# Kernel tuning notes

Hardware: AMD Instinct MI355X
Metric: run time of the kernel (lower is better)

The kernel has to match this reference:

```python
import jax, jax.numpy as jnp
import numpy as np

N = 100000
E = 640000
IN, HID, OUT = 128, 256, 128


def _glorot(key, shape):
    fan_in, fan_out = shape[0], shape[1]
    lim = (6.0 / (fan_in + fan_out)) ** 0.5
    return jax.random.uniform(key, shape, jnp.float32, -lim, lim)


def setup_inputs() -> dict:
    key = jax.random.key(0)
    ks = jax.random.split(key, 8)
    x = jax.random.normal(ks[0], (N, IN), jnp.float32)
    edge_index = jax.random.randint(ks[1], (2, E), 0, N, jnp.int64)
    # conv0 MLP: in->hid->hid
    w0a = _glorot(ks[2], (IN, HID)); b0a = jnp.zeros((HID,), jnp.float32)
    w0b = _glorot(ks[3], (HID, HID)); b0b = jnp.zeros((HID,), jnp.float32)
    # conv1 MLP: hid->hid->hid
    w1a = _glorot(ks[4], (HID, HID)); b1a = jnp.zeros((HID,), jnp.float32)
    w1b = _glorot(ks[5], (HID, HID)); b1b = jnp.zeros((HID,), jnp.float32)
    # conv2 MLP: hid->out->out
    w2a = _glorot(ks[6], (HID, OUT)); b2a = jnp.zeros((OUT,), jnp.float32)
    w2b = _glorot(ks[7], (OUT, OUT)); b2b = jnp.zeros((OUT,), jnp.float32)
    return dict(x=x, edge_index=edge_index,
                w0a=w0a, b0a=b0a, w0b=w0b, b0b=b0b,
                w1a=w1a, b1a=b1a, w1b=w1b, b1b=b1b,
                w2a=w2a, b2a=b2a, w2b=w2b, b2b=b2b)


def reference(x, edge_index, w0a, b0a, w0b, b0b, w1a, b1a, w1b, b1b, w2a, b2a, w2b, b2b):
    src, dst = edge_index[0], edge_index[1]
    n = x.shape[0]
    layers = [(w0a, b0a, w0b, b0b), (w1a, b1a, w1b, b1b), (w2a, b2a, w2b, b2b)]
    for wa, ba, wb, bb in layers:
        # GINConv (eps=0): aggregate neighbor messages x[src] into dst, add self
        agg = jax.ops.segment_sum(x[src], dst, num_segments=n)  # [N, d]
        h = x + agg
        h = jnp.maximum(h @ wa + ba, 0.0) @ wb + bb  # MLP: Linear-ReLU-Linear
        x = jnp.maximum(h, 0.0)  # outer F.relu
    return x
```

## Files before the change

kernel.cpp:

```cpp
#include <hip/hip_runtime.h>
#include <hip/hip_bf16.h>

typedef __attribute__((ext_vector_type(4))) float f32x4;
typedef __attribute__((ext_vector_type(8))) short short8;
typedef unsigned short u16;

__device__ inline float bf2f(u16 u) {
    unsigned int x = ((unsigned int)u) << 16;
    return __builtin_bit_cast(float, x);
}
__device__ inline u16 f2bf(float f) {
    unsigned int x = __builtin_bit_cast(unsigned int, f);
    unsigned int r = (x + 0x7FFFu + ((x >> 16) & 1u)) >> 16;
    return (u16)r;
}

__device__ inline int edge_at(const void* edges, int flag64, long long idx) {
    if (flag64) return (int)((const long long*)edges)[idx];
    return ((const int*)edges)[idx];
}

__global__ void probe_kernel(const void* edges, int n, int* flag) {
    if (threadIdx.x == 0 && blockIdx.x == 0) {
        const long long* p = (const long long*)edges;
        int ok = 1;
        for (int i = 0; i < 64; ++i) {
            long long v = p[i];
            if (v < 0 || v >= n) { ok = 0; break; }
        }
        *flag = ok;
    }
}

__global__ void hist_kernel(const void* edges, const int* flag, int E, int* deg) {
    int f = *flag;
    for (long long i = blockIdx.x * blockDim.x + threadIdx.x; i < E;
         i += (long long)gridDim.x * blockDim.x) {
        int dst = edge_at(edges, f, (long long)E + i);
        atomicAdd(&deg[dst], 1);
    }
}

__global__ void scan1_kernel(const int* deg, int* incl, int* bsum, int n) {
    __shared__ int s[256];
    int i = blockIdx.x * 256 + threadIdx.x;
    int v = (i < n) ? deg[i] : 0;
    s[threadIdx.x] = v;
    __syncthreads();
    for (int d = 1; d < 256; d <<= 1) {
        int t = (threadIdx.x >= d) ? s[threadIdx.x - d] : 0;
        __syncthreads();
        s[threadIdx.x] += t;
        __syncthreads();
    }
    if (i < n) incl[i] = s[threadIdx.x];
    if (threadIdx.x == 255) bsum[blockIdx.x] = s[255];
}

__global__ void scan2_kernel(const int* bsum, int* boff, int nb) {
    __shared__ int s[512];
    int t = threadIdx.x;
    int v = (t < nb) ? bsum[t] : 0;
    s[t] = v;
    __syncthreads();
    for (int d = 1; d < 512; d <<= 1) {
        int u = (t >= d) ? s[t - d] : 0;
        __syncthreads();
        s[t] += u;
        __syncthreads();
    }
    boff[t] = s[t] - v;
}

__global__ void scan3_kernel(const int* incl, const int* deg, const int* boff,
                             int* offs, int* cursor, int n, int E) {
    int i = blockIdx.x * 256 + threadIdx.x;
    if (i < n) {
        int o = boff[blockIdx.x] + incl[i] - deg[i];
        offs[i] = o;
        cursor[i] = o;
    }
    if (i == 0) offs[n] = E;
}

__global__ void scatter_kernel(const void* edges, const int* flag, int E,
                               int* cursor, int* nbr) {
    int f = *flag;
    for (long long i = blockIdx.x * blockDim.x + threadIdx.x; i < E;
         i += (long long)gridDim.x * blockDim.x) {
        int src = edge_at(edges, f, i);
        int dst = edge_at(edges, f, (long long)E + i);
        int pos = atomicAdd(&cursor[dst], 1);
        nbr[pos] = src;
    }
}

__global__ void cvt_x_kernel(const float* __restrict__ x, u16* __restrict__ out, long long n4) {
    long long i = blockIdx.x * blockDim.x + threadIdx.x;
    if (i >= n4) return;
    float4 v = ((const float4*)x)[i];
    ushort4 o;
    o.x = f2bf(v.x); o.y = f2bf(v.y); o.z = f2bf(v.z); o.w = f2bf(v.w);
    ((ushort4*)out)[i] = o;
}

__global__ void cvt_w_kernel(const float* __restrict__ W, u16* __restrict__ Wt, int K, int M) {
    int i = blockIdx.x * blockDim.x + threadIdx.x;
    if (i >= K * M) return;
    int m = i / K, k = i % K;
    Wt[i] = f2bf(W[(size_t)k * M + m]);
}

template <int FP>
__global__ __launch_bounds__(64) void agg_kernel(
    const u16* __restrict__ X, u16* __restrict__ H,
    const int* __restrict__ offs, const int* __restrict__ nbr, int n, int d) {
    const int node = blockIdx.x;
    const int lane = threadIdx.x;
    float acc[FP];
    const u16* xr = X + (size_t)node * d + lane * FP;
    if (FP == 2) {
        ushort2 v = *(const ushort2*)xr;
        acc[0] = bf2f(v.x); acc[1] = bf2f(v.y);
    } else {
        ushort4 v = *(const ushort4*)xr;
        acc[0] = bf2f(v.x); acc[1] = bf2f(v.y); acc[2] = bf2f(v.z); acc[3] = bf2f(v.w);
    }
    const int s = offs[node], e = offs[node + 1];
    int j = s;
    for (; j + 4 <= e; j += 4) {
        int n0 = nbr[j], n1 = nbr[j + 1], n2 = nbr[j + 2], n3 = nbr[j + 3];
        if (FP == 2) {
            ushort2 v0 = *(const ushort2*)(X + (size_t)n0 * d + lane * 2);
            ushort2 v1 = *(const ushort2*)(X + (size_t)n1 * d + lane * 2);
            ushort2 v2 = *(const ushort2*)(X + (size_t)n2 * d + lane * 2);
            ushort2 v3 = *(const ushort2*)(X + (size_t)n3 * d + lane * 2);
            acc[0] += bf2f(v0.x) + bf2f(v1.x) + bf2f(v2.x) + bf2f(v3.x);
            acc[1] += bf2f(v0.y) + bf2f(v1.y) + bf2f(v2.y) + bf2f(v3.y);
        } else {
            ushort4 v0 = *(const ushort4*)(X + (size_t)n0 * d + lane * 4);
            ushort4 v1 = *(const ushort4*)(X + (size_t)n1 * d + lane * 4);
            ushort4 v2 = *(const ushort4*)(X + (size_t)n2 * d + lane * 4);
            ushort4 v3 = *(const ushort4*)(X + (size_t)n3 * d + lane * 4);
            acc[0] += bf2f(v0.x) + bf2f(v1.x) + bf2f(v2.x) + bf2f(v3.x);
            acc[1] += bf2f(v0.y) + bf2f(v1.y) + bf2f(v2.y) + bf2f(v3.y);
            acc[2] += bf2f(v0.z) + bf2f(v1.z) + bf2f(v2.z) + bf2f(v3.z);
            acc[3] += bf2f(v0.w) + bf2f(v1.w) + bf2f(v2.w) + bf2f(v3.w);
        }
    }
    for (; j < e; ++j) {
        int nb = nbr[j];
        if (FP == 2) {
            ushort2 v = *(const ushort2*)(X + (size_t)nb * d + lane * 2);
            acc[0] += bf2f(v.x); acc[1] += bf2f(v.y);
        } else {
            ushort4 v = *(const ushort4*)(X + (size_t)nb * d + lane * 4);
            acc[0] += bf2f(v.x); acc[1] += bf2f(v.y); acc[2] += bf2f(v.z); acc[3] += bf2f(v.w);
        }
    }
    u16* hr = H + (size_t)node * d + lane * FP;
    if (FP == 2) {
        ushort2 o; o.x = f2bf(acc[0]); o.y = f2bf(acc[1]);
        *(ushort2*)hr = o;
    } else {
        ushort4 o; o.x = f2bf(acc[0]); o.y = f2bf(acc[1]); o.z = f2bf(acc[2]); o.w = f2bf(acc[3]);
        *(ushort4*)hr = o;
    }
}

__device__ inline f32x4 mfma16(short8 a, short8 b, f32x4 c) {
    return __builtin_amdgcn_mfma_f32_16x16x32_bf16(a, b, c, 0, 0, 0);
}

template <int K1, int M1, int M2, bool F32OUT>
__global__ __launch_bounds__(512, 2) void mlp_kernel(
    const u16* __restrict__ H,
    const u16* __restrict__ W1t,
    const float* __restrict__ b1,
    const u16* __restrict__ W2t,
    const float* __restrict__ b2,
    void* __restrict__ outp,
    int Nrows, int ntiles) {
    constexpr int S1 = K1 + 8;
    constexpr int S2 = M1 + 8;
    constexpr int SO = F32OUT ? (M2 + 4) : (M2 + 8);
    constexpr int OB = F32OUT ? 4 : 2;
    constexpr int NK1 = K1 / 32, NK2 = M1 / 32;
    constexpr int CW1 = M1 / 128, CW2 = M2 / 128;
    constexpr size_t LA = (size_t)64 * S1 * 2;
    constexpr size_t LT = (size_t)64 * S2 * 2;
    constexpr size_t LO = (size_t)64 * SO * OB;
    constexpr size_t LB = LA > LT ? (LA > LO ? LA : LO) : (LT > LO ? LT : LO);
    __shared__ __align__(16) char smem[LB];
    u16* bufA = (u16*)smem;
    u16* bufT = (u16*)smem;

    const int tid = threadIdx.x;
    const int lane = tid & 63;
    const int wid = tid >> 6;
    const int fl = lane & 15;
    const int kg = lane >> 4;
    const int rb = kg << 2;

    const int ws1 = wid * (M1 / 8);
    const int ws2 = wid * (M2 / 8);
    short8 w1f[CW1][NK1];
    short8 w2f[CW2][NK2];
    float bias1[CW1], bias2[CW2];
#pragma unroll
    for (int c = 0; c < CW1; ++c) {
        const u16* wp = W1t + (size_t)(ws1 + c * 16 + fl) * K1 + kg * 8;
        bias1[c] = b1[ws1 + c * 16 + fl];
#pragma unroll
        for (int kk = 0; kk < NK1; ++kk) w1f[c][kk] = *(const short8*)(wp + kk * 32);
    }
#pragma unroll
    for (int c = 0; c < CW2; ++c) {
        const u16* wp = W2t + (size_t)(ws2 + c * 16 + fl) * M1 + kg * 8;
        bias2[c] = b2[ws2 + c * 16 + fl];
#pragma unroll
        for (int kk = 0; kk < NK2; ++kk) w2f[c][kk] = *(const short8*)(wp + kk * 32);
    }

    constexpr int TPR = K1 / 8;
    constexpr int RPI = 512 / TPR;
    constexpr int NPASS = 64 / RPI;
    const int srow = tid / TPR;
    const int sce = (tid % TPR) * 8;

    uint4 apf[NPASS];
    auto load_tile = [&](int t) {
#pragma unroll
        for (int p = 0; p < NPASS; ++p) {
            apf[p] = make_uint4(0, 0, 0, 0);
            if (t < ntiles) {
                const int r = t * 64 + p * RPI + srow;
                if (r < Nrows) apf[p] = *(const uint4*)(H + (size_t)r * K1 + sce);
            }
        }
    };

    load_tile(blockIdx.x);

    for (int t = blockIdx.x; t < ntiles; t += gridDim.x) {
        const int r0 = t * 64;
#pragma unroll
        for (int p = 0; p < NPASS; ++p)
            *(uint4*)&bufA[(p * RPI + srow) * S1 + sce] = apf[p];
        __syncthreads();

        load_tile(t + gridDim.x);

        f32x4 acc[4][CW1];
#pragma unroll
        for (int m = 0; m < 4; ++m)
#pragma unroll
            for (int c = 0; c < CW1; ++c) acc[m][c] = (f32x4){0.f, 0.f, 0.f, 0.f};
#pragma unroll
        for (int kk = 0; kk < NK1; ++kk) {
            short8 a[4];
#pragma unroll
            for (int m = 0; m < 4; ++m)
                a[m] = *(const short8*)&bufA[(m * 16 + fl) * S1 + kk * 32 + kg * 8];
#pragma unroll
            for (int c = 0; c < CW1; ++c)
#pragma unroll
                for (int m = 0; m < 4; ++m) acc[m][c] = mfma16(a[m], w1f[c][kk], acc[m][c]);
        }
        __syncthreads();

#pragma unroll
        for (int c = 0; c < CW1; ++c) {
            const int col = ws1 + c * 16 + fl;
#pragma unroll
            for (int m = 0; m < 4; ++m)
#pragma unroll
                for (int j = 0; j < 4; ++j) {
                    float v = fmaxf(acc[m][c][j] + bias1[c], 0.f);
                    bufT[(m * 16 + rb + j) * S2 + col] = f2bf(v);
                }
        }
        __syncthreads();

        f32x4 acc2[4][CW2];
#pragma unroll
        for (int m = 0; m < 4; ++m)
#pragma unroll
            for (int c = 0; c < CW2; ++c) acc2[m][c] = (f32x4){0.f, 0.f, 0.f, 0.f};
#pragma unroll
        for (int kk = 0; kk < NK2; ++kk) {
            short8 a[4];
#pragma unroll
            for (int m = 0; m < 4; ++m)
                a[m] = *(const short8*)&bufT[(m * 16 + fl) * S2 + kk * 32 + kg * 8];
#pragma unroll
            for (int c = 0; c < CW2; ++c)
#pragma unroll
                for (int m = 0; m < 4; ++m) acc2[m][c] = mfma16(a[m], w2f[c][kk], acc2[m][c]);
        }
        __syncthreads();

#pragma unroll
        for (int c = 0; c < CW2; ++c) {
            const int col = ws2 + c * 16 + fl;
#pragma unroll
            for (int m = 0; m < 4; ++m)
#pragma unroll
                for (int j = 0; j < 4; ++j) {
                    float v = fmaxf(acc2[m][c][j] + bias2[c], 0.f);
                    const int row = m * 16 + rb + j;
                    if (F32OUT)
                        ((float*)smem)[row * SO + col] = v;
                    else
                        ((u16*)smem)[row * SO + col] = f2bf(v);
                }
        }
        __syncthreads();

        {
            constexpr int ROWB = M2 * OB;
            constexpr int TPRO = ROWB / 16;
            constexpr int RPIO = 512 / TPRO;
            const int orow = tid / TPRO;
            const int ocb = (tid % TPRO) * 16;
#pragma unroll
            for (int p = 0; p < 64 / RPIO; ++p) {
                const int row = p * RPIO + orow;
                if (r0 + row < Nrows) {
                    uint4 v = *(const uint4*)(smem + (size_t)row * SO * OB + ocb);
                    *(uint4*)((char*)outp + (size_t)(r0 + row) * ROWB + ocb) = v;
                }
            }
        }
        __syncthreads();
    }
}

extern "C" void kernel_launch(void* const* d_in, const int* in_sizes, int n_in,
                              void* d_out, int out_size, void* d_ws, size_t ws_size,
                              hipStream_t stream) {
    const int IN = 128, HID = 256, OUTD = 128;
    const int N = in_sizes[0] / IN;
    const int E = in_sizes[1] / 2;

    const float* x = (const float*)d_in[0];
    const void* edges = d_in[1];
    const float* w0a = (const float*)d_in[2];  const float* b0a = (const float*)d_in[3];
    const float* w0b = (const float*)d_in[4];  const float* b0b = (const float*)d_in[5];
    const float* w1a = (const float*)d_in[6];  const float* b1a = (const float*)d_in[7];
    const float* w1b = (const float*)d_in[8];  const float* b1b = (const float*)d_in[9];
    const float* w2a = (const float*)d_in[10]; const float* b2a = (const float*)d_in[11];
    const float* w2b = (const float*)d_in[12]; const float* b2b = (const float*)d_in[13];

    char* ws = (char*)d_ws;
    size_t off = 0;
    auto alloc = [&](size_t b) { size_t o = off; off = (off + b + 255) & ~(size_t)255; return o; };
    int* flag   = (int*)(ws + alloc(4));
    int* deg    = (int*)(ws + alloc((size_t)N * 4));
    int* incl   = (int*)(ws + alloc((size_t)N * 4));
    int* bsum   = (int*)(ws + alloc(512 * 4));
    int* boff   = (int*)(ws + alloc(512 * 4));
    int* offs   = (int*)(ws + alloc((size_t)(N + 1) * 4));
    int* cursor = (int*)(ws + alloc((size_t)N * 4));
    int* nbr    = (int*)(ws + alloc((size_t)E * 4));
    u16* wt0a = (u16*)(ws + alloc((size_t)IN * HID * 2));
    u16* wt0b = (u16*)(ws + alloc((size_t)HID * HID * 2));
    u16* wt1a = (u16*)(ws + alloc((size_t)HID * HID * 2));
    u16* wt1b = (u16*)(ws + alloc((size_t)HID * HID * 2));
    u16* wt2a = (u16*)(ws + alloc((size_t)HID * OUTD * 2));
    u16* wt2b = (u16*)(ws + alloc((size_t)OUTD * OUTD * 2));
    u16* Pa = (u16*)(ws + alloc((size_t)N * HID * 2));
    u16* Pb = (u16*)(ws + alloc((size_t)N * HID * 2));

    probe_kernel<<<1, 64, 0, stream>>>(edges, N, flag);
    hipMemsetAsync(deg, 0, (size_t)N * 4, stream);
    hist_kernel<<<2048, 256, 0, stream>>>(edges, flag, E, deg);
    int nb1 = (N + 255) / 256;
    scan1_kernel<<<nb1, 256, 0, stream>>>(deg, incl, bsum, N);
    scan2_kernel<<<1, 512, 0, stream>>>(bsum, boff, nb1);
    scan3_kernel<<<nb1, 256, 0, stream>>>(incl, deg, boff, offs, cursor, N, E);
    scatter_kernel<<<2048, 256, 0, stream>>>(edges, flag, E, cursor, nbr);

    long long n4 = (long long)N * IN / 4;
    cvt_x_kernel<<<(int)((n4 + 255) / 256), 256, 0, stream>>>(x, Pa, n4);
    cvt_w_kernel<<<(IN * HID + 255) / 256, 256, 0, stream>>>(w0a, wt0a, IN, HID);
    cvt_w_kernel<<<(HID * HID + 255) / 256, 256, 0, stream>>>(w0b, wt0b, HID, HID);
    cvt_w_kernel<<<(HID * HID + 255) / 256, 256, 0, stream>>>(w1a, wt1a, HID, HID);
    cvt_w_kernel<<<(HID * HID + 255) / 256, 256, 0, stream>>>(w1b, wt1b, HID, HID);
    cvt_w_kernel<<<(HID * OUTD + 255) / 256, 256, 0, stream>>>(w2a, wt2a, HID, OUTD);
    cvt_w_kernel<<<(OUTD * OUTD + 255) / 256, 256, 0, stream>>>(w2b, wt2b, OUTD, OUTD);

    const int ntiles = (N + 63) / 64;
    const int mgrid = ntiles < 512 ? ntiles : 512;

    agg_kernel<2><<<N, 64, 0, stream>>>(Pa, Pb, offs, nbr, N, IN);
    mlp_kernel<128, 256, 256, false><<<mgrid, 512, 0, stream>>>(Pb, wt0a, b0a, wt0b, b0b, Pa, N, ntiles);
    agg_kernel<4><<<N, 64, 0, stream>>>(Pa, Pb, offs, nbr, N, HID);
    mlp_kernel<256, 256, 256, false><<<mgrid, 512, 0, stream>>>(Pb, wt1a, b1a, wt1b, b1b, Pa, N, ntiles);
    agg_kernel<4><<<N, 64, 0, stream>>>(Pa, Pb, offs, nbr, N, HID);
    mlp_kernel<256, 128, 128, true><<<mgrid, 512, 0, stream>>>(Pb, wt2a, b2a, wt2b, b2b, d_out, N, ntiles);
}
```

Baseline: 371.5 us.

## Reorder last layer to apply linear before aggregation, separate LDS buffers

For the final GIN layer, the first linear (256->128) is applied before neighbor aggregation, using linearity of sum. The aggregation then gathers 128-wide rows instead of 256-wide and applies bias+ReLU itself, followed by a standalone second GEMM that writes f32 output. The MLP kernel also gets separate LDS regions for input, intermediate and output, which lets it drop several __syncthreads, at the cost of more dynamic shared memory and a grid halved to 256. This adds one launch and changes rounding order slightly, since the pre-aggregation GEMM output is stored in bf16.

```diff
diff --git a/kernel.cpp b/kernel.cpp
--- a/kernel.cpp
+++ b/kernel.cpp
@@ -111,10 +111,11 @@
     Wt[i] = f2bf(W[(size_t)k * M + m]);
 }
 
-template <int FP>
+template <int FP, bool BR>
 __global__ __launch_bounds__(64) void agg_kernel(
     const u16* __restrict__ X, u16* __restrict__ H,
-    const int* __restrict__ offs, const int* __restrict__ nbr, int n, int d) {
+    const int* __restrict__ offs, const int* __restrict__ nbr,
+    const float* __restrict__ bias, int n, int d) {
     const int node = blockIdx.x;
     const int lane = threadIdx.x;
     float acc[FP];
@@ -158,6 +159,11 @@
             acc[0] += bf2f(v.x); acc[1] += bf2f(v.y); acc[2] += bf2f(v.z); acc[3] += bf2f(v.w);
         }
     }
+    if (BR) {
+#pragma unroll
+        for (int q = 0; q < FP; ++q)
+            acc[q] = fmaxf(acc[q] + bias[lane * FP + q], 0.f);
+    }
     u16* hr = H + (size_t)node * d + lane * FP;
     if (FP == 2) {
         ushort2 o; o.x = f2bf(acc[0]); o.y = f2bf(acc[1]);
@@ -172,28 +178,22 @@
     return __builtin_amdgcn_mfma_f32_16x16x32_bf16(a, b, c, 0, 0, 0);
 }
 
-template <int K1, int M1, int M2, bool F32OUT>
+template <int K1, int M1, int M2>
 __global__ __launch_bounds__(512, 2) void mlp_kernel(
-    const u16* __restrict__ H,
-    const u16* __restrict__ W1t,
-    const float* __restrict__ b1,
-    const u16* __restrict__ W2t,
-    const float* __restrict__ b2,
-    void* __restrict__ outp,
-    int Nrows, int ntiles) {
+    const u16* __restrict__ H, const u16* __restrict__ W1t, const float* __restrict__ b1,
+    const u16* __restrict__ W2t, const float* __restrict__ b2,
+    u16* __restrict__ outp, int Nrows, int ntiles) {
     constexpr int S1 = K1 + 8;
-    constexpr int S2 = M1 + 8;
-    constexpr int SO = F32OUT ? (M2 + 4) : (M2 + 8);
-    constexpr int OB = F32OUT ? 4 : 2;
+    constexpr int S2 = M1 + 16;
+    constexpr int SO = M2 + 16;
     constexpr int NK1 = K1 / 32, NK2 = M1 / 32;
     constexpr int CW1 = M1 / 128, CW2 = M2 / 128;
     constexpr size_t LA = (size_t)64 * S1 * 2;
     constexpr size_t LT = (size_t)64 * S2 * 2;
-    constexpr size_t LO = (size_t)64 * SO * OB;
-    constexpr size_t LB = LA > LT ? (LA > LO ? LA : LO) : (LT > LO ? LT : LO);
-    __shared__ __align__(16) char smem[LB];
+    extern __shared__ char smem[];
     u16* bufA = (u16*)smem;
-    u16* bufT = (u16*)smem;
+    u16* bufT = (u16*)(smem + LA);
+    u16* bufO = (u16*)(smem + LA + LT);
 
     const int tid = threadIdx.x;
     const int lane = tid & 63;
@@ -267,7 +267,6 @@
 #pragma unroll
                 for (int m = 0; m < 4; ++m) acc[m][c] = mfma16(a[m], w1f[c][kk], acc[m][c]);
         }
-        __syncthreads();
 
 #pragma unroll
         for (int c = 0; c < CW1; ++c) {
@@ -298,7 +297,6 @@
 #pragma unroll
                 for (int m = 0; m < 4; ++m) acc2[m][c] = mfma16(a[m], w2f[c][kk], acc2[m][c]);
         }
-        __syncthreads();
 
 #pragma unroll
         for (int c = 0; c < CW2; ++c) {
@@ -308,17 +306,13 @@
 #pragma unroll
                 for (int j = 0; j < 4; ++j) {
                     float v = fmaxf(acc2[m][c][j] + bias2[c], 0.f);
-                    const int row = m * 16 + rb + j;
-                    if (F32OUT)
-                        ((float*)smem)[row * SO + col] = v;
-                    else
-                        ((u16*)smem)[row * SO + col] = f2bf(v);
+                    bufO[(m * 16 + rb + j) * SO + col] = f2bf(v);
                 }
         }
         __syncthreads();
 
         {
-            constexpr int ROWB = M2 * OB;
+            constexpr int ROWB = M2 * 2;
             constexpr int TPRO = ROWB / 16;
             constexpr int RPIO = 512 / TPRO;
             const int orow = tid / TPRO;
@@ -327,12 +321,126 @@
             for (int p = 0; p < 64 / RPIO; ++p) {
                 const int row = p * RPIO + orow;
                 if (r0 + row < Nrows) {
-                    uint4 v = *(const uint4*)(smem + (size_t)row * SO * OB + ocb);
+                    uint4 v = *(const uint4*)((char*)bufO + (size_t)row * SO * 2 + ocb);
                     *(uint4*)((char*)outp + (size_t)(r0 + row) * ROWB + ocb) = v;
                 }
             }
         }
-        __syncthreads();
+    }
+}
+
+template <int K, int M, bool BR, bool F32OUT>
+__global__ __launch_bounds__(512, 4) void gemm1_kernel(
+    const u16* __restrict__ H, const u16* __restrict__ Wt,
+    const float* __restrict__ bias, void* __restrict__ outp,
+    int Nrows, int ntiles) {
+    constexpr int S1 = K + 8;
+    constexpr int SO = F32OUT ? (M + 4) : (M + 16);
+    constexpr int OB = F32OUT ? 4 : 2;
+    constexpr int NK = K / 32;
+    constexpr int CW = M / 128;
+    constexpr size_t LA = (size_t)64 * S1 * 2;
+    extern __shared__ char smem[];
+    u16* bufA = (u16*)smem;
+    char* bufO = smem + LA;
+
+    const int tid = threadIdx.x;
+    const int lane = tid & 63;
+    const int wid = tid >> 6;
+    const int fl = lane & 15;
+    const int kg = lane >> 4;
+    const int rb = kg << 2;
+
+    const int ws = wid * (M / 8);
+    short8 wf[CW][NK];
+    float bs[CW];
+#pragma unroll
+    for (int c = 0; c < CW; ++c) {
+        const u16* wp = Wt + (size_t)(ws + c * 16 + fl) * K + kg * 8;
+        bs[c] = BR ? bias[ws + c * 16 + fl] : 0.f;
+#pragma unroll
+        for (int kk = 0; kk < NK; ++kk) wf[c][kk] = *(const short8*)(wp + kk * 32);
+    }
+
+    constexpr int TPR = K / 8;
+    constexpr int RPI = 512 / TPR;
+    constexpr int NPASS = 64 / RPI;
+    const int srow = tid / TPR;
+    const int sce = (tid % TPR) * 8;
+
+    uint4 apf[NPASS];
+    auto load_tile = [&](int t) {
+#pragma unroll
+        for (int p = 0; p < NPASS; ++p) {
+            apf[p] = make_uint4(0, 0, 0, 0);
+            if (t < ntiles) {
+                const int r = t * 64 + p * RPI + srow;
+                if (r < Nrows) apf[p] = *(const uint4*)(H + (size_t)r * K + sce);
+            }
+        }
+    };
+
+    load_tile(blockIdx.x);
+
+    for (int t = blockIdx.x; t < ntiles; t += gridDim.x) {
+        const int r0 = t * 64;
+#pragma unroll
+        for (int p = 0; p < NPASS; ++p)
+            *(uint4*)&bufA[(p * RPI + srow) * S1 + sce] = apf[p];
+        __syncthreads();
+
+        load_tile(t + gridDim.x);
+
+        f32x4 acc[4][CW];
+#pragma unroll
+        for (int m = 0; m < 4; ++m)
+#pragma unroll
+            for (int c = 0; c < CW; ++c) acc[m][c] = (f32x4){0.f, 0.f, 0.f, 0.f};
+#pragma unroll
+        for (int kk = 0; kk < NK; ++kk) {
+            short8 a[4];
+#pragma unroll
+            for (int m = 0; m < 4; ++m)
+                a[m] = *(const short8*)&bufA[(m * 16 + fl) * S1 + kk * 32 + kg * 8];
+#pragma unroll
+            for (int c = 0; c < CW; ++c)
+#pragma unroll
+                for (int m = 0; m < 4; ++m) acc[m][c] = mfma16(a[m], wf[c][kk], acc[m][c]);
+        }
+
+#pragma unroll
+        for (int c = 0; c < CW; ++c) {
+            const int col = ws + c * 16 + fl;
+#pragma unroll
+            for (int m = 0; m < 4; ++m)
+#pragma unroll
+                for (int j = 0; j < 4; ++j) {
+                    float v = acc[m][c][j];
+                    if (BR) v = fmaxf(v + bs[c], 0.f);
+                    const int row = m * 16 + rb + j;
+                    if (F32OUT)
+                        ((float*)bufO)[row * SO + col] = v;
+                    else
+                        ((u16*)bufO)[row * SO + col] = f2bf(v);
+                }
+        }
+        __syncthreads();
+
+        {
+            constexpr int ROWB = M * OB;
+            constexpr int TPRO = ROWB / 16;
+            constexpr int RPIO = 512 / TPRO;
+            const int orow = tid / TPRO;
+            const int ocb = (tid % TPRO) * 16;
+#pragma unroll
+            for (int p = 0; p < 64 / RPIO; ++p) {
+                const int row = p * RPIO + orow;
+                if (r0 + row < Nrows) {
+                    uint4 v = *(const uint4*)(bufO + (size_t)row * SO * OB + ocb);
+                    *(uint4*)((char*)outp + (size_t)(r0 + row) * ROWB + ocb) = v;
+                }
+            }
+        }
     }
 }
 
@@ -391,12 +499,19 @@
     cvt_w_kernel<<<(OUTD * OUTD + 255) / 256, 256, 0, stream>>>(w2b, wt2b, OUTD, OUTD);
 
     const int ntiles = (N + 63) / 64;
-    const int mgrid = ntiles < 512 ? ntiles : 512;
-
-    agg_kernel<2><<<N, 64, 0, stream>>>(Pa, Pb, offs, nbr, N, IN);
-    mlp_kernel<128, 256, 256, false><<<mgrid, 512, 0, stream>>>(Pb, wt0a, b0a, wt0b, b0b, Pa, N, ntiles);
-    agg_kernel<4><<<N, 64, 0, stream>>>(Pa, Pb, offs, nbr, N, HID);
-    mlp_kernel<256, 256, 256, false><<<mgrid, 512, 0, stream>>>(Pb, wt1a, b1a, wt1b, b1b, Pa, N, ntiles);
-    agg_kernel<4><<<N, 64, 0, stream>>>(Pa, Pb, offs, nbr, N, HID);
-    mlp_kernel<256, 128, 128, true><<<mgrid, 512, 0, stream>>>(Pb, wt2a, b2a, wt2b, b2b, d_out, N, ntiles);
-}
+    const int pgrid = ntiles < 256 ? ntiles : 256;
+    const int ggrid = ntiles < 512 ? ntiles : 512;
+
+    const size_t mlp_lds0 = (size_t)64 * (128 + 8) * 2 + (size_t)64 * (256 + 16) * 2 * 2;
+    const size_t mlp_lds1 = (size_t)64 * (256 + 8) * 2 + (size_t)64 * (256 + 16) * 2 * 2;
+    const size_t pre_lds  = (size_t)64 * (256 + 8) * 2 + (size_t)64 * (128 + 16) * 2;
+    const size_t fin_lds  = (size_t)64 * (128 + 8) * 2 + (size_t)64 * (128 + 4) * 4;
+
+    agg_kernel<2, false><<<N, 64, 0, stream>>>(Pa, Pb, offs, nbr, nullptr, N, IN);
+    mlp_kernel<128, 256, 256><<<pgrid, 512, mlp_lds0, stream>>>(Pb, wt0a, b0a, wt0b, b0b, Pa, N, ntiles);
+    agg_kernel<4, false><<<N, 64, 0, stream>>>(Pa, Pb, offs, nbr, nullptr, N, HID);
+    mlp_kernel<256, 256, 256><<<pgrid, 512, mlp_lds1, stream>>>(Pb, wt1a, b1a, wt1b, b1b, Pa, N, ntiles);
+    gemm1_kernel<256, 128, false, false><<<ggrid, 512, pre_lds, stream>>>(Pa, wt2a, nullptr, Pb, N, ntiles);
+    agg_kernel<2, true><<<N, 64, 0, stream>>>(Pb, Pa, offs, nbr, b2a, N, OUTD);
+    gemm1_kernel<128, 128, true, true><<<ggrid, 512, fin_lds, stream>>>(Pa, wt2b, b2b, d_out, N, ntiles);
+}
```

After: 341.4 us. -8.1%, faster.
